# Kernel optimization log

Measured on AMD Instinct MI355X. Metric: run time of the kernel, lower is better.

## Reference

```python
import jax, jax.numpy as jnp
import numpy as np

B, S, D, F, H, E, K = 4, 1024, 1024, 2048, 16, 8, 2
DK = D // H
LN_EPS = 1e-5


def setup_inputs() -> dict:
    key = jax.random.key(0)
    ks = jax.random.split(key, 32)
    rn = lambda k, shape, s=0.02: jax.random.normal(k, shape, jnp.float32) * s
    z = lambda shape: jnp.zeros(shape, jnp.float32)
    o = lambda shape: jnp.ones(shape, jnp.float32)
    return {
        "x": jax.random.normal(ks[0], (B, S, D), jnp.float32),
        "mask": jnp.ones((B, 1, S, S), jnp.int32),
        "wq1": rn(ks[1], (D, D)), "bq1": z(D), "wq2": rn(ks[2], (D, D)), "bq2": z(D),
        "wk1": rn(ks[3], (D, D)), "bk1": z(D), "wk2": rn(ks[4], (D, D)), "bk2": z(D),
        "wv1": rn(ks[5], (D, D)), "bv1": z(D), "wv2": rn(ks[6], (D, D)), "bv2": z(D),
        "wo": rn(ks[7], (D, D)), "bo": z(D),
        # layer norms
        "ln1_g": o(D), "ln1_b": z(D), "ln2_g": o(D), "ln2_b": z(D),
        "gate_w": rn(ks[8], (D, E)), "gate_b": z(E),
        "ew1": rn(ks[9], (E, D, F)), "eb1": z((E, F)),
        "ew2": rn(ks[10], (E, F, D)), "eb2": z((E, D)),
        "ew3": rn(ks[11], (E, D, F)), "eb3": z((E, F)),
    }


def _ln(x, g, b):
    m = jnp.mean(x, -1, keepdims=True)
    v = jnp.mean(jnp.square(x - m), -1, keepdims=True)
    return (x - m) * jax.lax.rsqrt(v + LN_EPS) * g + b


def _swiglu_proj(x, wa, ba, wb, bb):
    return jax.nn.silu(x @ wa + ba) * (x @ wb + bb)


def _heads(t, b, s):
    return t.reshape(b, s, H, DK).transpose(0, 2, 1, 3)  # [B,H,S,DK]


def reference(x, mask, wq1, bq1, wq2, bq2, wk1, bk1, wk2, bk2, wv1, bv1, wv2, bv2,
              wo, bo, ln1_g, ln1_b, ln2_g, ln2_b, gate_w, gate_b,
              ew1, eb1, ew2, eb2, ew3, eb3):
    b, s, d = x.shape
    # --- pre-norm self attention ---
    x2 = _ln(x, ln1_g, ln1_b)
    q = _heads(_swiglu_proj(x2, wq1, bq1, wq2, bq2), b, s)
    k = _heads(_swiglu_proj(x2, wk1, bk1, wk2, bk2), b, s)
    v = _heads(_swiglu_proj(x2, wv1, bv1, wv2, bv2), b, s)
    scores = jnp.einsum('bhqd,bhkd->bhqk', q, k) / np.sqrt(DK).astype(np.float32)
    scores = jnp.where(mask == 0, jnp.float32(-1e9), scores)
    attn = jax.nn.softmax(scores, axis=-1)
    ctx = jnp.einsum('bhqk,bhkd->bhqd', attn, v).transpose(0, 2, 1, 3).reshape(b, s, d)
    x = x + ctx @ wo + bo
    # --- pre-norm MoE SwiGLU FFN ---
    x2 = _ln(x, ln2_g, ln2_b)
    gate_probs = jax.nn.softmax(x2 @ gate_w + gate_b, axis=-1)          # [B,S,E]
    top_p, top_i = jax.lax.top_k(gate_probs, K)                          # [B,S,K]
    top_p = top_p / (jnp.sum(top_p, -1, keepdims=True) + 1e-6)
    # dense per-expert passes (math identical to masked loop in original:
    # expert(x*mask)*mask == expert(x) on selected tokens, 0 elsewhere)
    h = jax.nn.silu(jnp.einsum('bsd,edf->ebsf', x2, ew1) + eb1[:, None, None, :]) \
        * (jnp.einsum('bsd,edf->ebsf', x2, ew3) + eb3[:, None, None, :])
    eo = jnp.einsum('ebsf,efd->ebsd', h, ew2) + eb2[:, None, None, :]   # [E,B,S,D]
    comb = jnp.sum(jax.nn.one_hot(top_i, E, dtype=x.dtype) * top_p[..., None], axis=-2)  # [B,S,E]
    moe = jnp.einsum('ebsd,bse->bsd', eo, comb)
    return x + moe
```

## Files before the change

### kernel.cpp

```cpp
#include <hip/hip_runtime.h>
#include <math.h>

#define B_ 4
#define S_ 1024
#define D_ 1024
#define F_ 2048
#define H_ 16
#define E_ 8
#define DK_ 64
#define NTOK (B_*S_)

typedef unsigned short ushort_t;
typedef __attribute__((ext_vector_type(8))) short short8;
typedef __attribute__((ext_vector_type(4))) float floatx4;

__device__ __forceinline__ ushort_t f2bf(float f) {
    unsigned u = __float_as_uint(f);
    unsigned r = (u + 0x7fffu + ((u >> 16) & 1u)) >> 16;
    return (ushort_t)r;
}
__device__ __forceinline__ float bf2f(ushort_t h) {
    return __uint_as_float(((unsigned)h) << 16);
}

__device__ __forceinline__ void gload16(const void* g, void* l) {
    __builtin_amdgcn_global_load_lds(
        (const __attribute__((address_space(1))) unsigned*)g,
        (__attribute__((address_space(3))) unsigned*)l, 16, 0, 0);
}

__device__ __forceinline__ float blockReduceSum256(float v, volatile float* sred) {
    int tid = threadIdx.x;
    #pragma unroll
    for (int o = 32; o > 0; o >>= 1) v += __shfl_down(v, o, 64);
    __syncthreads();
    if ((tid & 63) == 0) sred[tid >> 6] = v;
    __syncthreads();
    return sred[0] + sred[1] + sred[2] + sred[3];
}

__global__ __launch_bounds__(256)
void ln_kernel(const float* __restrict__ x, const float* __restrict__ g,
               const float* __restrict__ b, ushort_t* __restrict__ yh) {
    __shared__ float sred[4];
    int row = blockIdx.x;
    int tid = threadIdx.x;
    const float* xr = x + (size_t)row * D_;
    float v[4];
    float s = 0.f;
    #pragma unroll
    for (int i = 0; i < 4; i++) { v[i] = xr[tid + 256*i]; s += v[i]; }
    float mean = blockReduceSum256(s, sred) * (1.f / D_);
    float s2 = 0.f;
    #pragma unroll
    for (int i = 0; i < 4; i++) { float d = v[i] - mean; s2 += d * d; }
    float var = blockReduceSum256(s2, sred) * (1.f / D_);
    float rstd = rsqrtf(var + 1e-5f);
    #pragma unroll
    for (int i = 0; i < 4; i++) {
        int c = tid + 256*i;
        float r = (v[i] - mean) * rstd * g[c] + b[c];
        yh[(size_t)row * D_ + c] = f2bf(r);
    }
}

__global__ __launch_bounds__(256)
void ln_gate_kernel(const float* __restrict__ x, const float* __restrict__ g,
                    const float* __restrict__ b, ushort_t* __restrict__ yh,
                    const float* __restrict__ gw, const float* __restrict__ gb,
                    int* __restrict__ tope, float2* __restrict__ topw) {
    __shared__ float sred[4];
    __shared__ float sgate[4][E_];
    int row = blockIdx.x;
    int tid = threadIdx.x;
    const float* xr = x + (size_t)row * D_;
    float v[4];
    float s = 0.f;
    #pragma unroll
    for (int i = 0; i < 4; i++) { v[i] = xr[tid + 256*i]; s += v[i]; }
    float mean = blockReduceSum256(s, sred) * (1.f / D_);
    float s2 = 0.f;
    #pragma unroll
    for (int i = 0; i < 4; i++) { float d = v[i] - mean; s2 += d * d; }
    float var = blockReduceSum256(s2, sred) * (1.f / D_);
    float rstd = rsqrtf(var + 1e-5f);

    float p[E_];
    #pragma unroll
    for (int e = 0; e < E_; e++) p[e] = 0.f;
    #pragma unroll
    for (int i = 0; i < 4; i++) {
        int c = tid + 256*i;
        float r = (v[i] - mean) * rstd * g[c] + b[c];
        yh[(size_t)row * D_ + c] = f2bf(r);
        const float* gwr = gw + (size_t)c * E_;
        #pragma unroll
        for (int e = 0; e < E_; e++) p[e] += r * gwr[e];
    }
    #pragma unroll
    for (int o = 32; o > 0; o >>= 1)
        #pragma unroll
        for (int e = 0; e < E_; e++) p[e] += __shfl_down(p[e], o, 64);
    __syncthreads();
    if ((tid & 63) == 0) {
        #pragma unroll
        for (int e = 0; e < E_; e++) sgate[tid >> 6][e] = p[e];
    }
    __syncthreads();
    if (tid == 0) {
        float q[E_];
        float mx = -1e30f;
        #pragma unroll
        for (int e = 0; e < E_; e++) {
            q[e] = sgate[0][e] + sgate[1][e] + sgate[2][e] + sgate[3][e] + gb[e];
            mx = fmaxf(mx, q[e]);
        }
        float sum = 0.f;
        #pragma unroll
        for (int e = 0; e < E_; e++) { q[e] = expf(q[e] - mx); sum += q[e]; }
        #pragma unroll
        for (int e = 0; e < E_; e++) q[e] /= sum;
        int i1 = 0;
        #pragma unroll
        for (int e = 1; e < E_; e++) if (q[e] > q[i1]) i1 = e;
        int i2 = (i1 == 0) ? 1 : 0;
        #pragma unroll
        for (int e = 0; e < E_; e++) if (e != i2 && e != i1 && q[e] > q[i2]) i2 = e;
        float denom = q[i1] + q[i2] + 1e-6f;
        tope[row] = i1 | (i2 << 8);
        topw[row] = make_float2(q[i1] / denom, q[i2] / denom);
    }
}

__global__ __launch_bounds__(256)
void build_lists(const int* __restrict__ tope, const float2* __restrict__ topw,
                 int* __restrict__ counts, int* __restrict__ offs,
                 int* __restrict__ idxl, float* __restrict__ wgtl)
{
    const int e = blockIdx.x;
    const int tid = threadIdx.x;
    const int lane = tid & 63, wv = tid >> 6;
    __shared__ int wsum[4];
    __shared__ int sbase;
    __shared__ int ctot[4][E_];
    if (tid == 0) sbase = 0;
    __syncthreads();
    int* il = idxl + (size_t)e * NTOK;
    float* wl = wgtl + (size_t)e * NTOK;
    int c8[E_];
    #pragma unroll
    for (int i = 0; i < E_; i++) c8[i] = 0;
    for (int t0 = 0; t0 < NTOK; t0 += 256) {
        int t = t0 + tid;
        int pk = tope[t];
        int i1 = pk & 255, i2 = (pk >> 8) & 255;
        #pragma unroll
        for (int i = 0; i < E_; i++) c8[i] += (i1 == i) + (i2 == i);
        bool m = (i1 == e) || (i2 == e);
        float2 wp = topw[t];
        float w = (i1 == e) ? wp.x : wp.y;
        unsigned long long mask = __ballot(m);
        int wpos = __popcll(mask & ((1ull << lane) - 1ull));
        int wcnt = __popcll(mask);
        if (lane == 0) wsum[wv] = wcnt;
        __syncthreads();
        int base = sbase;
        int pre = 0;
        #pragma unroll
        for (int i = 0; i < 4; i++) if (i < wv) pre += wsum[i];
        if (m) { il[base + pre + wpos] = t; wl[base + pre + wpos] = w; }
        __syncthreads();
        if (tid == 0) sbase = base + wsum[0] + wsum[1] + wsum[2] + wsum[3];
    }
    #pragma unroll
    for (int i = 0; i < E_; i++)
        #pragma unroll
        for (int o = 32; o > 0; o >>= 1) c8[i] += __shfl_down(c8[i], o, 64);
    if (lane == 0) {
        #pragma unroll
        for (int i = 0; i < E_; i++) ctot[wv][i] = c8[i];
    }
    __syncthreads();
    if (tid == 0) {
        int off = 0;
        for (int i = 0; i < e; i++)
            off += ctot[0][i] + ctot[1][i] + ctot[2][i] + ctot[3][i];
        offs[e] = off;
        counts[e] = sbase;
    }
}

struct W7 { const float* s[7]; ushort_t* d[7]; };
__global__ __launch_bounds__(256)
void transpose7(W7 p, int R, int C)
{
    const float* s = p.s[blockIdx.z];
    ushort_t* d = p.d[blockIdx.z];
    __shared__ float t[32][33];
    int r0 = blockIdx.y * 32, c0 = blockIdx.x * 32;
    int lr = threadIdx.x >> 3, lc = (threadIdx.x & 7) * 4;
    float4 v = *(const float4*)(s + (size_t)(r0 + lr) * C + c0 + lc);
    t[lr][lc+0] = v.x; t[lr][lc+1] = v.y; t[lr][lc+2] = v.z; t[lr][lc+3] = v.w;
    __syncthreads();
    ushort4 o;
    o.x = f2bf(t[lc+0][lr]); o.y = f2bf(t[lc+1][lr]);
    o.z = f2bf(t[lc+2][lr]); o.w = f2bf(t[lc+3][lr]);
    *(ushort4*)(d + (size_t)(c0 + lr) * R + r0 + lc) = o;
}

__global__ __launch_bounds__(256)
void transpose_e13(const float* __restrict__ ew1, const float* __restrict__ ew3,
                   ushort_t* __restrict__ e1t, ushort_t* __restrict__ e3t)
{
    const int z = blockIdx.z;
    const int e = z >> 1, which = z & 1;
    const float* s = (which ? ew3 : ew1) + (size_t)e * D_ * F_;
    ushort_t* d = (which ? e3t : e1t) + (size_t)e * D_ * F_;
    const int R = D_, C = F_;
    int r0 = blockIdx.y * 32, c0 = blockIdx.x * 32;
    __shared__ float t[32][33];
    int lr = threadIdx.x >> 3, lc = (threadIdx.x & 7) * 4;
    float4 v = *(const float4*)(s + (size_t)(r0 + lr) * C + c0 + lc);
    t[lr][lc+0] = v.x; t[lr][lc+1] = v.y; t[lr][lc+2] = v.z; t[lr][lc+3] = v.w;
    __syncthreads();
    ushort4 o;
    o.x = f2bf(t[lc+0][lr]); o.y = f2bf(t[lc+1][lr]);
    o.z = f2bf(t[lc+2][lr]); o.w = f2bf(t[lc+3][lr]);
    *(ushort4*)(d + (size_t)(c0 + lr) * R + r0 + lc) = o;
}

__global__ __launch_bounds__(256)
void transpose_e2(const float* __restrict__ ew2, ushort_t* __restrict__ e2t)
{
    const int e = blockIdx.z;
    const float* s = ew2 + (size_t)e * F_ * D_;
    ushort_t* d = e2t + (size_t)e * F_ * D_;
    const int R = F_, C = D_;
    int r0 = blockIdx.y * 32, c0 = blockIdx.x * 32;
    __shared__ float t[32][33];
    int lr = threadIdx.x >> 3, lc = (threadIdx.x & 7) * 4;
    float4 v = *(const float4*)(s + (size_t)(r0 + lr) * C + c0 + lc);
    t[lr][lc+0] = v.x; t[lr][lc+1] = v.y; t[lr][lc+2] = v.z; t[lr][lc+3] = v.w;
    __syncthreads();
    ushort4 o;
    o.x = f2bf(t[lc+0][lr]); o.y = f2bf(t[lc+1][lr]);
    o.z = f2bf(t[lc+2][lr]); o.w = f2bf(t[lc+3][lr]);
    *(ushort4*)(d + (size_t)(c0 + lr) * R + r0 + lc) = o;
}

__global__ __launch_bounds__(256)
void mgemm_res(const ushort_t* __restrict__ A, const ushort_t* __restrict__ B1,
               const float* __restrict__ bias1, const float* __restrict__ R,
               float* __restrict__ Cv, int M, int N, int K)
{
    __shared__ __align__(16) ushort_t As [128*32];
    __shared__ __align__(16) ushort_t Bs1[128*32];

    int tid = threadIdx.x;
    int m0 = blockIdx.y * 128, n0 = blockIdx.x * 128;
    int trow = tid >> 2;
    int tcol = (tid & 3) * 8;
    const ushort_t* gA  = A  + (size_t)(m0 + trow) * K + tcol;
    const ushort_t* gB1 = B1 + (size_t)(n0 + trow) * K + tcol;
    ushort_t* lA  = &As [trow*32 + tcol];
    ushort_t* lB1 = &Bs1[trow*32 + tcol];

    int wave = tid >> 6, lane = tid & 63;
    int wm = (wave >> 1) * 64, wn = (wave & 1) * 64;
    int fr = lane & 15, fk = (lane >> 4) * 8;
    const ushort_t* pa  = &As [(wm + fr)*32 + fk];
    const ushort_t* pb1 = &Bs1[(wn + fr)*32 + fk];

    floatx4 acc1[4][4];
    #pragma unroll
    for (int i = 0; i < 4; i++)
        #pragma unroll
        for (int j = 0; j < 4; j++) acc1[i][j] = (floatx4)(0.f);

    for (int k0 = 0; k0 < K; k0 += 32) {
        gload16(gA  + k0,            lA);
        gload16(gA  + (size_t)64*K + k0, lA  + 64*32);
        gload16(gB1 + k0,            lB1);
        gload16(gB1 + (size_t)64*K + k0, lB1 + 64*32);
        __syncthreads();

        short8 a[4];
        #pragma unroll
        for (int mt = 0; mt < 4; mt++) a[mt] = *(const short8*)(pa + mt*16*32);
        short8 b[4];
        #pragma unroll
        for (int nt = 0; nt < 4; nt++) b[nt] = *(const short8*)(pb1 + nt*16*32);
        #pragma unroll
        for (int mt = 0; mt < 4; mt++)
            #pragma unroll
            for (int nt = 0; nt < 4; nt++)
                acc1[mt][nt] = __builtin_amdgcn_mfma_f32_16x16x32_bf16(
                    a[mt], b[nt], acc1[mt][nt], 0, 0, 0);
        __syncthreads();
    }

    int ecol0 = n0 + wn + (lane & 15);
    int erow0 = m0 + wm + (lane >> 4) * 4;
    #pragma unroll
    for (int mt = 0; mt < 4; mt++) {
        #pragma unroll
        for (int nt = 0; nt < 4; nt++) {
            int col = ecol0 + nt * 16;
            #pragma unroll
            for (int r = 0; r < 4; r++) {
                int row = erow0 + mt * 16 + r;
                size_t idx = (size_t)row * N + col;
                Cv[idx] = acc1[mt][nt][r] + bias1[col] + R[idx];
            }
        }
    }
}

struct QKV {
    const ushort_t* B1[3]; const ushort_t* B2[3];
    const float* bias1[3]; const float* bias2[3];
    ushort_t* C[3];
};
__global__ __launch_bounds__(256)
void mgemm_qkv(const ushort_t* __restrict__ A, QKV p)
{
    const int z = blockIdx.z;
    const ushort_t* B1 = p.B1[z];
    const ushort_t* B2 = p.B2[z];
    const float* bias1 = p.bias1[z];
    const float* bias2 = p.bias2[z];
    ushort_t* C = p.C[z];
    const int N = D_, K = D_;

    __shared__ __align__(16) ushort_t As [128*32];
    __shared__ __align__(16) ushort_t Bs1[128*32];
    __shared__ __align__(16) ushort_t Bs2[128*32];

    int tid = threadIdx.x;
    int m0 = blockIdx.y * 128, n0 = blockIdx.x * 128;
    int trow = tid >> 2;
    int tcol = (tid & 3) * 8;
    const ushort_t* gA  = A  + (size_t)(m0 + trow) * K + tcol;
    const ushort_t* gB1 = B1 + (size_t)(n0 + trow) * K + tcol;
    const ushort_t* gB2 = B2 + (size_t)(n0 + trow) * K + tcol;
    ushort_t* lA  = &As [trow*32 + tcol];
    ushort_t* lB1 = &Bs1[trow*32 + tcol];
    ushort_t* lB2 = &Bs2[trow*32 + tcol];

    int wave = tid >> 6, lane = tid & 63;
    int wm = (wave >> 1) * 64, wn = (wave & 1) * 64;
    int fr = lane & 15, fk = (lane >> 4) * 8;
    const ushort_t* pa  = &As [(wm + fr)*32 + fk];
    const ushort_t* pb1 = &Bs1[(wn + fr)*32 + fk];
    const ushort_t* pb2 = &Bs2[(wn + fr)*32 + fk];

    floatx4 acc1[4][4], acc2[4][4];
    #pragma unroll
    for (int i = 0; i < 4; i++)
        #pragma unroll
        for (int j = 0; j < 4; j++) { acc1[i][j] = (floatx4)(0.f); acc2[i][j] = (floatx4)(0.f); }

    for (int k0 = 0; k0 < K; k0 += 32) {
        gload16(gA  + k0,            lA);
        gload16(gA  + (size_t)64*K + k0, lA  + 64*32);
        gload16(gB1 + k0,            lB1);
        gload16(gB1 + (size_t)64*K + k0, lB1 + 64*32);
        gload16(gB2 + k0,            lB2);
        gload16(gB2 + (size_t)64*K + k0, lB2 + 64*32);
        __syncthreads();

        short8 a[4];
        #pragma unroll
        for (int mt = 0; mt < 4; mt++) a[mt] = *(const short8*)(pa + mt*16*32);
        {
            short8 b[4];
            #pragma unroll
            for (int nt = 0; nt < 4; nt++) b[nt] = *(const short8*)(pb1 + nt*16*32);
            #pragma unroll
            for (int mt = 0; mt < 4; mt++)
                #pragma unroll
                for (int nt = 0; nt < 4; nt++)
                    acc1[mt][nt] = __builtin_amdgcn_mfma_f32_16x16x32_bf16(
                        a[mt], b[nt], acc1[mt][nt], 0, 0, 0);
        }
        {
            short8 b[4];
            #pragma unroll
            for (int nt = 0; nt < 4; nt++) b[nt] = *(const short8*)(pb2 + nt*16*32);
            #pragma unroll
            for (int mt = 0; mt < 4; mt++)
                #pragma unroll
                for (int nt = 0; nt < 4; nt++)
                    acc2[mt][nt] = __builtin_amdgcn_mfma_f32_16x16x32_bf16(
                        a[mt], b[nt], acc2[mt][nt], 0, 0, 0);
        }
        __syncthreads();
    }

    int ecol0 = n0 + wn + (lane & 15);
    int erow0 = m0 + wm + (lane >> 4) * 4;
    #pragma unroll
    for (int mt = 0; mt < 4; mt++) {
        #pragma unroll
        for (int nt = 0; nt < 4; nt++) {
            int col = ecol0 + nt * 16;
            #pragma unroll
            for (int r = 0; r < 4; r++) {
                int row = erow0 + mt * 16 + r;
                float x1 = acc1[mt][nt][r] + bias1[col];
                float x2 = acc2[mt][nt][r] + bias2[col];
                float h = x1 / (1.f + __expf(-x1)) * x2;
                C[(size_t)row * N + col] = f2bf(h);
            }
        }
    }
}

__global__ __launch_bounds__(256)
void mgemm_up_all(const ushort_t* __restrict__ A, const int* __restrict__ idxl_all,
                  const int* __restrict__ counts, const int* __restrict__ offs,
                  const ushort_t* __restrict__ B1a, const float* __restrict__ b1a,
                  const ushort_t* __restrict__ B2a, const float* __restrict__ b2a,
                  ushort_t* __restrict__ Call)
{
    const int e = blockIdx.z;
    int cnt = counts[e];
    int m0 = blockIdx.y * 128;
    if (m0 >= cnt) return;
    const int N = F_, K = D_;
    const int* idxl = idxl_all + (size_t)e * NTOK;
    const ushort_t* B1 = B1a + (size_t)e * D_ * F_;
    const ushort_t* B2 = B2a + (size_t)e * D_ * F_;
    const float* bias1 = b1a + (size_t)e * F_;
    const float* bias2 = b2a + (size_t)e * F_;
    ushort_t* C = Call + (size_t)offs[e] * F_;

    __shared__ __align__(16) ushort_t As [128*32];
    __shared__ __align__(16) ushort_t Bs1[128*32];
    __shared__ __align__(16) ushort_t Bs2[128*32];

    int tid = threadIdx.x;
    int n0 = blockIdx.x * 128;
    int trow = tid >> 2;
    int tcol = (tid & 3) * 8;
    int r0 = m0 + trow, r1 = m0 + 64 + trow;
    int t0 = (r0 < cnt) ? idxl[r0] : 0;
    int t1 = (r1 < cnt) ? idxl[r1] : 0;
    const ushort_t* gA0 = A + (size_t)t0 * K + tcol;
    const ushort_t* gA1 = A + (size_t)t1 * K + tcol;
    const ushort_t* gB1 = B1 + (size_t)(n0 + trow) * K + tcol;
    const ushort_t* gB2 = B2 + (size_t)(n0 + trow) * K + tcol;
    ushort_t* lA  = &As [trow*32 + tcol];
    ushort_t* lB1 = &Bs1[trow*32 + tcol];
    ushort_t* lB2 = &Bs2[trow*32 + tcol];

    int wave = tid >> 6, lane = tid & 63;
    int wm = (wave >> 1) * 64, wn = (wave & 1) * 64;
    int fr = lane & 15, fk = (lane >> 4) * 8;
    const ushort_t* pa  = &As [(wm + fr)*32 + fk];
    const ushort_t* pb1 = &Bs1[(wn + fr)*32 + fk];
    const ushort_t* pb2 = &Bs2[(wn + fr)*32 + fk];

    floatx4 acc1[4][4], acc2[4][4];
    #pragma unroll
    for (int i = 0; i < 4; i++)
        #pragma unroll
        for (int j = 0; j < 4; j++) { acc1[i][j] = (floatx4)(0.f); acc2[i][j] = (floatx4)(0.f); }

    for (int k0 = 0; k0 < K; k0 += 32) {
        gload16(gA0 + k0, lA);
        gload16(gA1 + k0, lA + 64*32);
        gload16(gB1 + k0, lB1);
        gload16(gB1 + (size_t)64*K + k0, lB1 + 64*32);
        gload16(gB2 + k0, lB2);
        gload16(gB2 + (size_t)64*K + k0, lB2 + 64*32);
        __syncthreads();

        short8 a[4];
        #pragma unroll
        for (int mt = 0; mt < 4; mt++) a[mt] = *(const short8*)(pa + mt*16*32);
        {
            short8 b[4];
            #pragma unroll
            for (int nt = 0; nt < 4; nt++) b[nt] = *(const short8*)(pb1 + nt*16*32);
            #pragma unroll
            for (int mt = 0; mt < 4; mt++)
                #pragma unroll
                for (int nt = 0; nt < 4; nt++)
                    acc1[mt][nt] = __builtin_amdgcn_mfma_f32_16x16x32_bf16(
                        a[mt], b[nt], acc1[mt][nt], 0, 0, 0);
        }
        {
            short8 b[4];
            #pragma unroll
            for (int nt = 0; nt < 4; nt++) b[nt] = *(const short8*)(pb2 + nt*16*32);
            #pragma unroll
            for (int mt = 0; mt < 4; mt++)
                #pragma unroll
                for (int nt = 0; nt < 4; nt++)
                    acc2[mt][nt] = __builtin_amdgcn_mfma_f32_16x16x32_bf16(
                        a[mt], b[nt], acc2[mt][nt], 0, 0, 0);
        }
        __syncthreads();
    }

    int ecol0 = n0 + wn + (lane & 15);
    int erow0 = m0 + wm + (lane >> 4) * 4;
    #pragma unroll
    for (int mt = 0; mt < 4; mt++) {
        #pragma unroll
        for (int nt = 0; nt < 4; nt++) {
            int col = ecol0 + nt * 16;
            #pragma unroll
            for (int r = 0; r < 4; r++) {
                int row = erow0 + mt * 16 + r;
                if (row < cnt) {
                    float x1 = acc1[mt][nt][r] + bias1[col];
                    float x2 = acc2[mt][nt][r] + bias2[col];
                    float h = x1 / (1.f + __expf(-x1)) * x2;
                    C[(size_t)row * N + col] = f2bf(h);
                }
            }
        }
    }
}

__global__ __launch_bounds__(256)
void mgemm_down_all(const ushort_t* __restrict__ hA, const int* __restrict__ idxl_all,
                    const float* __restrict__ wgtl_all, const int* __restrict__ counts,
                    const int* __restrict__ offs, const ushort_t* __restrict__ B1a,
                    const float* __restrict__ b1a, float* __restrict__ out)
{
    const int e = blockIdx.z;
    int cnt = counts[e];
    int m0 = blockIdx.y * 128;
    if (m0 >= cnt) return;
    const int N = D_, K = F_;
    const int* idxl = idxl_all + (size_t)e * NTOK;
    const float* wgtl = wgtl_all + (size_t)e * NTOK;
    const ushort_t* A = hA + (size_t)offs[e] * F_;
    const ushort_t* B1 = B1a + (size_t)e * F_ * D_;
    const float* bias1 = b1a + (size_t)e * D_;

    __shared__ __align__(16) ushort_t As [128*32];
    __shared__ __align__(16) ushort_t Bs1[128*32];

    int tid = threadIdx.x;
    int n0 = blockIdx.x * 128;
    int trow = tid >> 2;
    int tcol = (tid & 3) * 8;
    const ushort_t* gA  = A  + (size_t)(m0 + trow) * K + tcol;
    const ushort_t* gB1 = B1 + (size_t)(n0 + trow) * K + tcol;
    ushort_t* lA  = &As [trow*32 + tcol];
    ushort_t* lB1 = &Bs1[trow*32 + tcol];

    int wave = tid >> 6, lane = tid & 63;
    int wm = (wave >> 1) * 64, wn = (wave & 1) * 64;
    int fr = lane & 15, fk = (lane >> 4) * 8;
    const ushort_t* pa  = &As [(wm + fr)*32 + fk];
    const ushort_t* pb1 = &Bs1[(wn + fr)*32 + fk];

    floatx4 acc1[4][4];
    #pragma unroll
    for (int i = 0; i < 4; i++)
        #pragma unroll
        for (int j = 0; j < 4; j++) acc1[i][j] = (floatx4)(0.f);

    for (int k0 = 0; k0 < K; k0 += 32) {
        gload16(gA + k0,             lA);
        gload16(gA + (size_t)64*K + k0, lA + 64*32);
        gload16(gB1 + k0,            lB1);
        gload16(gB1 + (size_t)64*K + k0, lB1 + 64*32);
        __syncthreads();

        short8 a[4];
        #pragma unroll
        for (int mt = 0; mt < 4; mt++) a[mt] = *(const short8*)(pa + mt*16*32);
        short8 b[4];
        #pragma unroll
        for (int nt = 0; nt < 4; nt++) b[nt] = *(const short8*)(pb1 + nt*16*32);
        #pragma unroll
        for (int mt = 0; mt < 4; mt++)
            #pragma unroll
            for (int nt = 0; nt < 4; nt++)
                acc1[mt][nt] = __builtin_amdgcn_mfma_f32_16x16x32_bf16(
                    a[mt], b[nt], acc1[mt][nt], 0, 0, 0);
        __syncthreads();
    }

    int ecol0 = n0 + wn + (lane & 15);
    int erow0 = m0 + wm + (lane >> 4) * 4;
    #pragma unroll
    for (int mt = 0; mt < 4; mt++) {
        int rowb = erow0 + mt * 16;
        int tok[4]; float wv[4];
        #pragma unroll
        for (int r = 0; r < 4; r++) {
            int row = rowb + r;
            tok[r] = (row < cnt) ? idxl[row] : -1;
            wv[r]  = (row < cnt) ? wgtl[row] : 0.f;
        }
        #pragma unroll
        for (int nt = 0; nt < 4; nt++) {
            int col = ecol0 + nt * 16;
            #pragma unroll
            for (int r = 0; r < 4; r++) {
                if (tok[r] >= 0)
                    atomicAdd(&out[(size_t)tok[r] * N + col],
                              wv[r] * (acc1[mt][nt][r] + bias1[col]));
            }
        }
    }
}

__global__ __launch_bounds__(256)
void fattn_kernel(const ushort_t* __restrict__ q, const ushort_t* __restrict__ k,
                  const ushort_t* __restrict__ v, ushort_t* __restrict__ ctx)
{
    __shared__ __align__(16) ushort_t Ks[64*72];
    __shared__ __align__(16) ushort_t Vt[64*72];
    __shared__ __align__(16) ushort_t Ps[4][16*72];

    const int bid = blockIdx.x;
    const int qt = bid & (S_/64 - 1);
    const int h  = (bid >> 4) & (H_ - 1);
    const int b  = bid >> 8;
    const int tid = threadIdx.x;
    const int wave = tid >> 6, lane = tid & 63;
    const int RS = H_ * DK_;
    const size_t headbase = ((size_t)b * S_ * H_ + h) * DK_;
    const int s0 = qt * 64;
    const int lr = lane & 15, lg = lane >> 4;

    short8 qf0, qf1;
    {
        const ushort_t* qp = q + headbase + (size_t)(s0 + wave*16 + lr) * RS + lg * 8;
        qf0 = *(const short8*)qp;
        qf1 = *(const short8*)(qp + 32);
    }

    floatx4 O[4];
    float m_i[4], l_i[4];
    #pragma unroll
    for (int i = 0; i < 4; i++) { O[i] = (floatx4)(0.f); m_i[i] = -1e30f; l_i[i] = 0.f; }

    const int kr = tid >> 3, kc = (tid & 7) * 8;
    ushort_t* pw = Ps[wave];

    for (int t = 0; t < S_/64; t++) {
        const int kbase = t * 64;
        __syncthreads();
        {
            const ushort_t* kp = k + headbase + (size_t)(kbase + kr) * RS + kc;
            short8 k0 = *(const short8*)kp;
            short8 k1 = *(const short8*)(kp + (size_t)32 * RS);
            *(short8*)&Ks[kr*72 + kc]        = k0;
            *(short8*)&Ks[(kr + 32)*72 + kc] = k1;
        }
        {
            const ushort_t* vp = v + headbase + (size_t)(kbase + wave*16) * RS + lane;
            short8 w0, w1;
            #pragma unroll
            for (int j = 0; j < 8; j++) {
                ((ushort_t*)&w0)[j] = vp[(size_t)j * RS];
                ((ushort_t*)&w1)[j] = vp[(size_t)(j + 8) * RS];
            }
            *(short8*)&Vt[lane*72 + wave*16]     = w0;
            *(short8*)&Vt[lane*72 + wave*16 + 8] = w1;
        }
        __syncthreads();

        floatx4 sacc[4];
        #pragma unroll
        for (int nt = 0; nt < 4; nt++) sacc[nt] = (floatx4)(0.f);
        #pragma unroll
        for (int nt = 0; nt < 4; nt++) {
            short8 b0 = *(const short8*)&Ks[(lr + nt*16)*72 + lg*8];
            sacc[nt] = __builtin_amdgcn_mfma_f32_16x16x32_bf16(qf0, b0, sacc[nt], 0, 0, 0);
            short8 b1 = *(const short8*)&Ks[(lr + nt*16)*72 + 32 + lg*8];
            sacc[nt] = __builtin_amdgcn_mfma_f32_16x16x32_bf16(qf1, b1, sacc[nt], 0, 0, 0);
        }

        float alpha[4];
        #pragma unroll
        for (int r = 0; r < 4; r++) {
            float rm = -1e30f;
            #pragma unroll
            for (int nt = 0; nt < 4; nt++) { sacc[nt][r] *= 0.125f; rm = fmaxf(rm, sacc[nt][r]); }
            #pragma unroll
            for (int o = 1; o < 16; o <<= 1) rm = fmaxf(rm, __shfl_xor(rm, o, 64));
            float nm = fmaxf(m_i[r], rm);
            alpha[r] = __expf(m_i[r] - nm);
            m_i[r] = nm;
            float rs = 0.f;
            #pragma unroll
            for (int nt = 0; nt < 4; nt++) { sacc[nt][r] = __expf(sacc[nt][r] - nm); rs += sacc[nt][r]; }
            #pragma unroll
            for (int o = 1; o < 16; o <<= 1) rs += __shfl_xor(rs, o, 64);
            l_i[r] = l_i[r] * alpha[r] + rs;
        }

        #pragma unroll
        for (int nt = 0; nt < 4; nt++)
            #pragma unroll
            for (int r = 0; r < 4; r++)
                pw[(lg*4 + r)*72 + lr + nt*16] = f2bf(sacc[nt][r]);

        #pragma unroll
        for (int nt = 0; nt < 4; nt++)
            #pragma unroll
            for (int r = 0; r < 4; r++)
                O[nt][r] *= alpha[r];

        asm volatile("s_waitcnt lgkmcnt(0)" ::: "memory");

        #pragma unroll
        for (int kh = 0; kh < 2; kh++) {
            short8 pa = *(const short8*)&pw[lr*72 + kh*32 + lg*8];
            #pragma unroll
            for (int nt = 0; nt < 4; nt++) {
                short8 bv = *(const short8*)&Vt[(lr + nt*16)*72 + kh*32 + lg*8];
                O[nt] = __builtin_amdgcn_mfma_f32_16x16x32_bf16(pa, bv, O[nt], 0, 0, 0);
            }
        }
    }

    #pragma unroll
    for (int r = 0; r < 4; r++) {
        float inv = 1.f / l_i[r];
        #pragma unroll
        for (int nt = 0; nt < 4; nt++)
            pw[(lg*4 + r)*72 + lr + nt*16] = f2bf(O[nt][r] * inv);
    }
    asm volatile("s_waitcnt lgkmcnt(0)" ::: "memory");
    {
        const int row = lane >> 2, c0 = (lane & 3) * 16;
        short8 o0 = *(const short8*)&pw[row*72 + c0];
        short8 o1 = *(const short8*)&pw[row*72 + c0 + 8];
        ushort_t* gp = ctx + headbase + (size_t)(s0 + wave*16 + row) * RS + c0;
        *(short8*)gp       = o0;
        *(short8*)(gp + 8) = o1;
    }
}

extern "C" void kernel_launch(void* const* d_in, const int* in_sizes, int n_in,
                              void* d_out, int out_size, void* d_ws, size_t ws_size,
                              hipStream_t stream)
{
    const float* x    = (const float*)d_in[0];
    const float* wq1  = (const float*)d_in[2];
    const float* bq1  = (const float*)d_in[3];
    const float* wq2  = (const float*)d_in[4];
    const float* bq2  = (const float*)d_in[5];
    const float* wk1  = (const float*)d_in[6];
    const float* bk1  = (const float*)d_in[7];
    const float* wk2  = (const float*)d_in[8];
    const float* bk2  = (const float*)d_in[9];
    const float* wv1  = (const float*)d_in[10];
    const float* bv1  = (const float*)d_in[11];
    const float* wv2  = (const float*)d_in[12];
    const float* bv2  = (const float*)d_in[13];
    const float* wo   = (const float*)d_in[14];
    const float* bo   = (const float*)d_in[15];
    const float* ln1g = (const float*)d_in[16];
    const float* ln1b = (const float*)d_in[17];
    const float* ln2g = (const float*)d_in[18];
    const float* ln2b = (const float*)d_in[19];
    const float* gw   = (const float*)d_in[20];
    const float* gb   = (const float*)d_in[21];
    const float* ew1  = (const float*)d_in[22];
    const float* eb1  = (const float*)d_in[23];
    const float* ew2  = (const float*)d_in[24];
    const float* eb2  = (const float*)d_in[25];
    const float* ew3  = (const float*)d_in[26];
    const float* eb3  = (const float*)d_in[27];
    float* out = (float*)d_out;

    const size_t MB = 1024ull * 1024ull;
    char* w = (char*)d_ws;
    ushort_t* wq1t = (ushort_t*)(w +  0*MB);
    ushort_t* wq2t = (ushort_t*)(w +  2*MB);
    ushort_t* wk1t = (ushort_t*)(w +  4*MB);
    ushort_t* wk2t = (ushort_t*)(w +  6*MB);
    ushort_t* wv1t = (ushort_t*)(w +  8*MB);
    ushort_t* wv2t = (ushort_t*)(w + 10*MB);
    ushort_t* wot  = (ushort_t*)(w + 12*MB);
    ushort_t* x2h  = (ushort_t*)(w + 14*MB);
    ushort_t* qh   = (ushort_t*)(w + 22*MB);
    ushort_t* kh   = (ushort_t*)(w + 30*MB);
    ushort_t* vh   = (ushort_t*)(w + 38*MB);
    ushort_t* ctxh = (ushort_t*)(w + 46*MB);
    ushort_t* e1t  = (ushort_t*)(w +  0*MB);
    ushort_t* e3t  = (ushort_t*)(w + 32*MB);
    ushort_t* e2t  = (ushort_t*)(w +  0*MB);
    ushort_t* x2bh = (ushort_t*)(w + 64*MB);
    ushort_t* hAh  = (ushort_t*)(w + 72*MB);
    char* tail = w + 105*MB;
    int*    cnts = (int*)tail;     tail += 256;
    int*    offs = (int*)tail;     tail += 256;
    int*    idxl = (int*)tail;     tail += (size_t)E_ * NTOK * 4;
    float*  wgtl = (float*)tail;   tail += (size_t)E_ * NTOK * 4;
    int*    tope = (int*)tail;     tail += (size_t)NTOK * 4;
    float2* topw = (float2*)tail;  tail += (size_t)NTOK * 8;

    dim3 blk(256);

    W7 p7;
    p7.s[0]=wq1; p7.d[0]=wq1t; p7.s[1]=wq2; p7.d[1]=wq2t;
    p7.s[2]=wk1; p7.d[2]=wk1t; p7.s[3]=wk2; p7.d[3]=wk2t;
    p7.s[4]=wv1; p7.d[4]=wv1t; p7.s[5]=wv2; p7.d[5]=wv2t;
    p7.s[6]=wo;  p7.d[6]=wot;
    transpose7<<<dim3(32,32,7), blk, 0, stream>>>(p7, D_, D_);

    ln_kernel<<<NTOK, blk, 0, stream>>>(x, ln1g, ln1b, x2h);
    QKV qp;
    qp.B1[0]=wq1t; qp.B2[0]=wq2t; qp.bias1[0]=bq1; qp.bias2[0]=bq2; qp.C[0]=qh;
    qp.B1[1]=wk1t; qp.B2[1]=wk2t; qp.bias1[1]=bk1; qp.bias2[1]=bk2; qp.C[1]=kh;
    qp.B1[2]=wv1t; qp.B2[2]=wv2t; qp.bias1[2]=bv1; qp.bias2[2]=bv2; qp.C[2]=vh;
    mgemm_qkv<<<dim3(D_/128, NTOK/128, 3), blk, 0, stream>>>(x2h, qp);
    fattn_kernel<<<B_ * H_ * (S_/64), blk, 0, stream>>>(qh, kh, vh, ctxh);
    mgemm_res<<<dim3(D_/128, NTOK/128), blk, 0, stream>>>(ctxh, wot, bo, x, out,
                                                          NTOK, D_, D_);

    ln_gate_kernel<<<NTOK, blk, 0, stream>>>(out, ln2g, ln2b, x2bh, gw, gb,
                                             tope, topw);
    build_lists<<<dim3(E_), blk, 0, stream>>>(tope, topw, cnts, offs, idxl, wgtl);
    transpose_e13<<<dim3(F_/32, D_/32, 2*E_), blk, 0, stream>>>(ew1, ew3, e1t, e3t);
    mgemm_up_all<<<dim3(F_/128, NTOK/128, E_), blk, 0, stream>>>(
        x2bh, idxl, cnts, offs, e1t, eb1, e3t, eb3, hAh);
    transpose_e2<<<dim3(D_/32, F_/32, E_), blk, 0, stream>>>(ew2, e2t);
    mgemm_down_all<<<dim3(D_/128, NTOK/128, E_), blk, 0, stream>>>(
        hAh, idxl, wgtl, cnts, offs, e2t, eb2, out);
}
```

Measured before the change: 867.4 us.

## Double-buffer LDS tiles in all MFMA GEMM kernels to overlap loads with compute

Each GEMM kernel now keeps two shared-memory tile buffers and prefetches the next K-slice into the idle buffer while MFMAs consume the current one, with a prologue load before the loop. This removes one barrier per iteration and aims to hide global memory latency behind matrix math. It doubles LDS usage per block, which may lower occupancy, and raises register pressure.

```diff
diff --git a/kernel.cpp b/kernel.cpp
--- a/kernel.cpp
+++ b/kernel.cpp
@@ -253,8 +253,8 @@
                const float* __restrict__ bias1, const float* __restrict__ R,
                float* __restrict__ Cv, int M, int N, int K)
 {
-    __shared__ __align__(16) ushort_t As [128*32];
-    __shared__ __align__(16) ushort_t Bs1[128*32];
+    __shared__ __align__(16) ushort_t As [2][128*32];
+    __shared__ __align__(16) ushort_t Bs1[2][128*32];
 
     int tid = threadIdx.x;
     int m0 = blockIdx.y * 128, n0 = blockIdx.x * 128;
@@ -262,14 +262,13 @@
     int tcol = (tid & 3) * 8;
     const ushort_t* gA  = A  + (size_t)(m0 + trow) * K + tcol;
     const ushort_t* gB1 = B1 + (size_t)(n0 + trow) * K + tcol;
-    ushort_t* lA  = &As [trow*32 + tcol];
-    ushort_t* lB1 = &Bs1[trow*32 + tcol];
+    const int lofs = trow*32 + tcol;
 
     int wave = tid >> 6, lane = tid & 63;
     int wm = (wave >> 1) * 64, wn = (wave & 1) * 64;
     int fr = lane & 15, fk = (lane >> 4) * 8;
-    const ushort_t* pa  = &As [(wm + fr)*32 + fk];
-    const ushort_t* pb1 = &Bs1[(wn + fr)*32 + fk];
+    const int pofsA = (wm + fr)*32 + fk;
+    const int pofsB = (wn + fr)*32 + fk;
 
     floatx4 acc1[4][4];
     #pragma unroll
@@ -277,19 +276,27 @@
         #pragma unroll
         for (int j = 0; j < 4; j++) acc1[i][j] = (floatx4)(0.f);
 
+    gload16(gA,                  &As [0][lofs]);
+    gload16(gA  + (size_t)64*K,  &As [0][lofs + 64*32]);
+    gload16(gB1,                 &Bs1[0][lofs]);
+    gload16(gB1 + (size_t)64*K,  &Bs1[0][lofs + 64*32]);
+    __syncthreads();
+
+    int cur = 0;
     for (int k0 = 0; k0 < K; k0 += 32) {
-        gload16(gA  + k0,            lA);
-        gload16(gA  + (size_t)64*K + k0, lA  + 64*32);
-        gload16(gB1 + k0,            lB1);
-        gload16(gB1 + (size_t)64*K + k0, lB1 + 64*32);
-        __syncthreads();
-
+        int nxt = cur ^ 1;
+        if (k0 + 32 < K) {
+            gload16(gA  + k0 + 32,                 &As [nxt][lofs]);
+            gload16(gA  + (size_t)64*K + k0 + 32,  &As [nxt][lofs + 64*32]);
+            gload16(gB1 + k0 + 32,                 &Bs1[nxt][lofs]);
+            gload16(gB1 + (size_t)64*K + k0 + 32,  &Bs1[nxt][lofs + 64*32]);
+        }
         short8 a[4];
         #pragma unroll
-        for (int mt = 0; mt < 4; mt++) a[mt] = *(const short8*)(pa + mt*16*32);
+        for (int mt = 0; mt < 4; mt++) a[mt] = *(const short8*)&As[cur][pofsA + mt*16*32];
         short8 b[4];
         #pragma unroll
-        for (int nt = 0; nt < 4; nt++) b[nt] = *(const short8*)(pb1 + nt*16*32);
+        for (int nt = 0; nt < 4; nt++) b[nt] = *(const short8*)&Bs1[cur][pofsB + nt*16*32];
         #pragma unroll
         for (int mt = 0; mt < 4; mt++)
             #pragma unroll
@@ -297,6 +304,7 @@
                 acc1[mt][nt] = __builtin_amdgcn_mfma_f32_16x16x32_bf16(
                     a[mt], b[nt], acc1[mt][nt], 0, 0, 0);
         __syncthreads();
+        cur = nxt;
     }
 
     int ecol0 = n0 + wn + (lane & 15);
@@ -332,9 +340,9 @@
     ushort_t* C = p.C[z];
     const int N = D_, K = D_;
 
-    __shared__ __align__(16) ushort_t As [128*32];
-    __shared__ __align__(16) ushort_t Bs1[128*32];
-    __shared__ __align__(16) ushort_t Bs2[128*32];
+    __shared__ __align__(16) ushort_t As [2][128*32];
+    __shared__ __align__(16) ushort_t Bs1[2][128*32];
+    __shared__ __align__(16) ushort_t Bs2[2][128*32];
 
     int tid = threadIdx.x;
     int m0 = blockIdx.y * 128, n0 = blockIdx.x * 128;
@@ -343,16 +351,13 @@
     const ushort_t* gA  = A  + (size_t)(m0 + trow) * K + tcol;
     const ushort_t* gB1 = B1 + (size_t)(n0 + trow) * K + tcol;
     const ushort_t* gB2 = B2 + (size_t)(n0 + trow) * K + tcol;
-    ushort_t* lA  = &As [trow*32 + tcol];
-    ushort_t* lB1 = &Bs1[trow*32 + tcol];
-    ushort_t* lB2 = &Bs2[trow*32 + tcol];
+    const int lofs = trow*32 + tcol;
 
     int wave = tid >> 6, lane = tid & 63;
     int wm = (wave >> 1) * 64, wn = (wave & 1) * 64;
     int fr = lane & 15, fk = (lane >> 4) * 8;
-    const ushort_t* pa  = &As [(wm + fr)*32 + fk];
-    const ushort_t* pb1 = &Bs1[(wn + fr)*32 + fk];
-    const ushort_t* pb2 = &Bs2[(wn + fr)*32 + fk];
+    const int pofsA = (wm + fr)*32 + fk;
+    const int pofsB = (wn + fr)*32 + fk;
 
     floatx4 acc1[4][4], acc2[4][4];
     #pragma unroll
@@ -360,22 +365,32 @@
         #pragma unroll
         for (int j = 0; j < 4; j++) { acc1[i][j] = (floatx4)(0.f); acc2[i][j] = (floatx4)(0.f); }
 
+    gload16(gA,                  &As [0][lofs]);
+    gload16(gA  + (size_t)64*K,  &As [0][lofs + 64*32]);
+    gload16(gB1,                 &Bs1[0][lofs]);
+    gload16(gB1 + (size_t)64*K,  &Bs1[0][lofs + 64*32]);
+    gload16(gB2,                 &Bs2[0][lofs]);
+    gload16(gB2 + (size_t)64*K,  &Bs2[0][lofs + 64*32]);
+    __syncthreads();
+
+    int cur = 0;
     for (int k0 = 0; k0 < K; k0 += 32) {
-        gload16(gA  + k0,            lA);
-        gload16(gA  + (size_t)64*K + k0, lA  + 64*32);
-        gload16(gB1 + k0,            lB1);
-        gload16(gB1 + (size_t)64*K + k0, lB1 + 64*32);
-        gload16(gB2 + k0,            lB2);
-        gload16(gB2 + (size_t)64*K + k0, lB2 + 64*32);
-        __syncthreads();
-
+        int nxt = cur ^ 1;
+        if (k0 + 32 < K) {
+            gload16(gA  + k0 + 32,                 &As [nxt][lofs]);
+            gload16(gA  + (size_t)64*K + k0 + 32,  &As [nxt][lofs + 64*32]);
+            gload16(gB1 + k0 + 32,                 &Bs1[nxt][lofs]);
+            gload16(gB1 + (size_t)64*K + k0 + 32,  &Bs1[nxt][lofs + 64*32]);
+            gload16(gB2 + k0 + 32,                 &Bs2[nxt][lofs]);
+            gload16(gB2 + (size_t)64*K + k0 + 32,  &Bs2[nxt][lofs + 64*32]);
+        }
         short8 a[4];
         #pragma unroll
-        for (int mt = 0; mt < 4; mt++) a[mt] = *(const short8*)(pa + mt*16*32);
+        for (int mt = 0; mt < 4; mt++) a[mt] = *(const short8*)&As[cur][pofsA + mt*16*32];
         {
             short8 b[4];
             #pragma unroll
-            for (int nt = 0; nt < 4; nt++) b[nt] = *(const short8*)(pb1 + nt*16*32);
+            for (int nt = 0; nt < 4; nt++) b[nt] = *(const short8*)&Bs1[cur][pofsB + nt*16*32];
             #pragma unroll
             for (int mt = 0; mt < 4; mt++)
                 #pragma unroll
@@ -386,7 +401,7 @@
         {
             short8 b[4];
             #pragma unroll
-            for (int nt = 0; nt < 4; nt++) b[nt] = *(const short8*)(pb2 + nt*16*32);
+            for (int nt = 0; nt < 4; nt++) b[nt] = *(const short8*)&Bs2[cur][pofsB + nt*16*32];
             #pragma unroll
             for (int mt = 0; mt < 4; mt++)
                 #pragma unroll
@@ -395,6 +410,7 @@
                         a[mt], b[nt], acc2[mt][nt], 0, 0, 0);
         }
         __syncthreads();
+        cur = nxt;
     }
 
     int ecol0 = n0 + wn + (lane & 15);
@@ -435,9 +451,9 @@
     const float* bias2 = b2a + (size_t)e * F_;
     ushort_t* C = Call + (size_t)offs[e] * F_;
 
-    __shared__ __align__(16) ushort_t As [128*32];
-    __shared__ __align__(16) ushort_t Bs1[128*32];
-    __shared__ __align__(16) ushort_t Bs2[128*32];
+    __shared__ __align__(16) ushort_t As [2][128*32];
+    __shared__ __align__(16) ushort_t Bs1[2][128*32];
+    __shared__ __align__(16) ushort_t Bs2[2][128*32];
 
     int tid = threadIdx.x;
     int n0 = blockIdx.x * 128;
@@ -450,16 +466,13 @@
     const ushort_t* gA1 = A + (size_t)t1 * K + tcol;
     const ushort_t* gB1 = B1 + (size_t)(n0 + trow) * K + tcol;
     const ushort_t* gB2 = B2 + (size_t)(n0 + trow) * K + tcol;
-    ushort_t* lA  = &As [trow*32 + tcol];
-    ushort_t* lB1 = &Bs1[trow*32 + tcol];
-    ushort_t* lB2 = &Bs2[trow*32 + tcol];
+    const int lofs = trow*32 + tcol;
 
     int wave = tid >> 6, lane = tid & 63;
     int wm = (wave >> 1) * 64, wn = (wave & 1) * 64;
     int fr = lane & 15, fk = (lane >> 4) * 8;
-    const ushort_t* pa  = &As [(wm + fr)*32 + fk];
-    const ushort_t* pb1 = &Bs1[(wn + fr)*32 + fk];
-    const ushort_t* pb2 = &Bs2[(wn + fr)*32 + fk];
+    const int pofsA = (wm + fr)*32 + fk;
+    const int pofsB = (wn + fr)*32 + fk;
 
     floatx4 acc1[4][4], acc2[4][4];
     #pragma unroll
@@ -467,22 +480,32 @@
         #pragma unroll
         for (int j = 0; j < 4; j++) { acc1[i][j] = (floatx4)(0.f); acc2[i][j] = (floatx4)(0.f); }
 
+    gload16(gA0,                 &As [0][lofs]);
+    gload16(gA1,                 &As [0][lofs + 64*32]);
+    gload16(gB1,                 &Bs1[0][lofs]);
+    gload16(gB1 + (size_t)64*K,  &Bs1[0][lofs + 64*32]);
+    gload16(gB2,                 &Bs2[0][lofs]);
+    gload16(gB2 + (size_t)64*K,  &Bs2[0][lofs + 64*32]);
+    __syncthreads();
+
+    int cur = 0;
     for (int k0 = 0; k0 < K; k0 += 32) {
-        gload16(gA0 + k0, lA);
-        gload16(gA1 + k0, lA + 64*32);
-        gload16(gB1 + k0, lB1);
-        gload16(gB1 + (size_t)64*K + k0, lB1 + 64*32);
-        gload16(gB2 + k0, lB2);
-        gload16(gB2 + (size_t)64*K + k0, lB2 + 64*32);
-        __syncthreads();
-
+        int nxt = cur ^ 1;
+        if (k0 + 32 < K) {
+            gload16(gA0 + k0 + 32,                 &As [nxt][lofs]);
+            gload16(gA1 + k0 + 32,                 &As [nxt][lofs + 64*32]);
+            gload16(gB1 + k0 + 32,                 &Bs1[nxt][lofs]);
+            gload16(gB1 + (size_t)64*K + k0 + 32,  &Bs1[nxt][lofs + 64*32]);
+            gload16(gB2 + k0 + 32,                 &Bs2[nxt][lofs]);
+            gload16(gB2 + (size_t)64*K + k0 + 32,  &Bs2[nxt][lofs + 64*32]);
+        }
         short8 a[4];
         #pragma unroll
-        for (int mt = 0; mt < 4; mt++) a[mt] = *(const short8*)(pa + mt*16*32);
+        for (int mt = 0; mt < 4; mt++) a[mt] = *(const short8*)&As[cur][pofsA + mt*16*32];
         {
             short8 b[4];
             #pragma unroll
-            for (int nt = 0; nt < 4; nt++) b[nt] = *(const short8*)(pb1 + nt*16*32);
+            for (int nt = 0; nt < 4; nt++) b[nt] = *(const short8*)&Bs1[cur][pofsB + nt*16*32];
             #pragma unroll
             for (int mt = 0; mt < 4; mt++)
                 #pragma unroll
@@ -493,7 +516,7 @@
         {
             short8 b[4];
             #pragma unroll
-            for (int nt = 0; nt < 4; nt++) b[nt] = *(const short8*)(pb2 + nt*16*32);
+            for (int nt = 0; nt < 4; nt++) b[nt] = *(const short8*)&Bs2[cur][pofsB + nt*16*32];
             #pragma unroll
             for (int mt = 0; mt < 4; mt++)
                 #pragma unroll
@@ -502,6 +525,7 @@
                         a[mt], b[nt], acc2[mt][nt], 0, 0, 0);
         }
         __syncthreads();
+        cur = nxt;
     }
 
     int ecol0 = n0 + wn + (lane & 15);
@@ -542,8 +566,8 @@
     const ushort_t* B1 = B1a + (size_t)e * F_ * D_;
     const float* bias1 = b1a + (size_t)e * D_;
 
-    __shared__ __align__(16) ushort_t As [128*32];
-    __shared__ __align__(16) ushort_t Bs1[128*32];
+    __shared__ __align__(16) ushort_t As [2][128*32];
+    __shared__ __align__(16) ushort_t Bs1[2][128*32];
 
     int tid = threadIdx.x;
     int n0 = blockIdx.x * 128;
@@ -551,14 +575,13 @@
     int tcol = (tid & 3) * 8;
     const ushort_t* gA  = A  + (size_t)(m0 + trow) * K + tcol;
     const ushort_t* gB1 = B1 + (size_t)(n0 + trow) * K + tcol;
-    ushort_t* lA  = &As [trow*32 + tcol];
-    ushort_t* lB1 = &Bs1[trow*32 + tcol];
+    const int lofs = trow*32 + tcol;
 
     int wave = tid >> 6, lane = tid & 63;
     int wm = (wave >> 1) * 64, wn = (wave & 1) * 64;
     int fr = lane & 15, fk = (lane >> 4) * 8;
-    const ushort_t* pa  = &As [(wm + fr)*32 + fk];
-    const ushort_t* pb1 = &Bs1[(wn + fr)*32 + fk];
+    const int pofsA = (wm + fr)*32 + fk;
+    const int pofsB = (wn + fr)*32 + fk;
 
     floatx4 acc1[4][4];
     #pragma unroll
@@ -566,19 +589,27 @@
         #pragma unroll
         for (int j = 0; j < 4; j++) acc1[i][j] = (floatx4)(0.f);
 
+    gload16(gA,                  &As [0][lofs]);
+    gload16(gA  + (size_t)64*K,  &As [0][lofs + 64*32]);
+    gload16(gB1,                 &Bs1[0][lofs]);
+    gload16(gB1 + (size_t)64*K,  &Bs1[0][lofs + 64*32]);
+    __syncthreads();
+
+    int cur = 0;
     for (int k0 = 0; k0 < K; k0 += 32) {
-        gload16(gA + k0,             lA);
-        gload16(gA + (size_t)64*K + k0, lA + 64*32);
-        gload16(gB1 + k0,            lB1);
-        gload16(gB1 + (size_t)64*K + k0, lB1 + 64*32);
-        __syncthreads();
-
+        int nxt = cur ^ 1;
+        if (k0 + 32 < K) {
+            gload16(gA  + k0 + 32,                 &As [nxt][lofs]);
+            gload16(gA  + (size_t)64*K + k0 + 32,  &As [nxt][lofs + 64*32]);
+            gload16(gB1 + k0 + 32,                 &Bs1[nxt][lofs]);
+            gload16(gB1 + (size_t)64*K + k0 + 32,  &Bs1[nxt][lofs + 64*32]);
+        }
         short8 a[4];
         #pragma unroll
-        for (int mt = 0; mt < 4; mt++) a[mt] = *(const short8*)(pa + mt*16*32);
+        for (int mt = 0; mt < 4; mt++) a[mt] = *(const short8*)&As[cur][pofsA + mt*16*32];
         short8 b[4];
         #pragma unroll
-        for (int nt = 0; nt < 4; nt++) b[nt] = *(const short8*)(pb1 + nt*16*32);
+        for (int nt = 0; nt < 4; nt++) b[nt] = *(const short8*)&Bs1[cur][pofsB + nt*16*32];
         #pragma unroll
         for (int mt = 0; mt < 4; mt++)
             #pragma unroll
@@ -586,6 +617,7 @@
                 acc1[mt][nt] = __builtin_amdgcn_mfma_f32_16x16x32_bf16(
                     a[mt], b[nt], acc1[mt][nt], 0, 0, 0);
         __syncthreads();
+        cur = nxt;
     }
 
     int ecol0 = n0 + wn + (lane & 15);
```

Result: faster. 745.1 us (-14.1%).
